# Kernel optimization log

Hardware: AMD Instinct MI355X
Metric: run time of the kernel (lower is better)

## Reference

```python
import jax, jax.numpy as jnp
import numpy as np

B, S, H, D = 2, 2048, 16, 128
HID = H * D  # 2048


def _quantum(x, real, imag, phase, mag):
    # |x * e^{i*phase} * (real + i*imag) * mag| == |x| * sqrt(real^2+imag^2) * |mag|
    # (phase has unit modulus, so it drops out of the magnitude; grad wrt phase is 0,
    # matching torch.abs of the complex product.)
    return jnp.abs(x) * jnp.sqrt(real * real + imag * imag) * jnp.abs(mag)


def setup_inputs() -> dict:
    key = jax.random.key(0)
    ks = jax.random.split(key, 20)
    p = lambda i, shape, s=0.02: jax.random.normal(ks[i], shape, dtype=jnp.float32) * s
    inp = {
        "hidden_states": jax.random.normal(ks[0], (B, S, HID), dtype=jnp.float32),
        "attention_mask": jnp.zeros((B, 1, 1, S), dtype=jnp.float32),
    }
    i = 1
    for name in ("q", "k", "v"):
        inp[name + "_real"] = p(i, (HID,)); i += 1
        inp[name + "_imag"] = p(i, (HID,)); i += 1
        inp[name + "_phase"] = p(i, (HID,), 0.1); i += 1
        inp[name + "_mag"] = jnp.ones((HID,), dtype=jnp.float32)
    for name in ("q", "k", "v", "o"):
        inp["W" + name] = p(i, (HID, HID)); i += 1  # torch Linear weight [out, in]
        inp["b" + name] = jnp.zeros((HID,), dtype=jnp.float32)
    inp["ent"] = p(i, (H, H))
    return inp


def reference(hidden_states, attention_mask,
              q_real, q_imag, q_phase, q_mag,
              k_real, k_imag, k_phase, k_mag,
              v_real, v_imag, v_phase, v_mag,
              Wq, bq, Wk, bk, Wv, bv, Wo, bo, ent):
    Bsz, Sl, _ = hidden_states.shape

    def heads(x):  # [B,S,HID] -> [B,H,S,D]
        return x.reshape(Bsz, Sl, H, D).transpose(0, 2, 1, 3)

    q = heads(_quantum(hidden_states @ Wq.T + bq, q_real, q_imag, q_phase, q_mag))
    k = heads(_quantum(hidden_states @ Wk.T + bk, k_real, k_imag, k_phase, k_mag))
    v = heads(_quantum(hidden_states @ Wv.T + bv, v_real, v_imag, v_phase, v_mag))

    scores = jnp.einsum('bhsd,bhtd->bhst', q, k) / jnp.sqrt(jnp.float32(D))
    # entanglement bias: [H,H] tiled along key axis -> [1,H,1,S]
    bias = jnp.tile(ent, (1, Sl // H))[None, :, None, :]
    scores = scores + bias + attention_mask
    probs = jax.nn.softmax(scores, axis=-1)

    ctx = jnp.einsum('bhst,bhtd->bhsd', probs, v)
    ctx = ctx.transpose(0, 2, 1, 3).reshape(Bsz, Sl, HID)
    return ctx @ Wo.T + bo
```

## Files before the change

kernel.cpp:

```cpp
#include <hip/hip_runtime.h>
#include <hip/hip_bf16.h>

#define NB 2
#define NS 2048
#define NH 16
#define ND 128
#define HID2 2048
#define MROWS 4096

typedef __bf16 bf16;
typedef bf16 bf16x8 __attribute__((ext_vector_type(8)));
typedef bf16 bf16x4 __attribute__((ext_vector_type(4)));
typedef float f32x4 __attribute__((ext_vector_type(4)));
typedef unsigned int u32;

#define GLOBAL_AS __attribute__((address_space(1)))
#define LDS_AS __attribute__((address_space(3)))

__device__ __forceinline__ void async16(void* lds, const void* g) {
    __builtin_amdgcn_global_load_lds((const GLOBAL_AS u32*)g, (LDS_AS u32*)lds, 16, 0, 0);
}

__device__ __forceinline__ void cvt8(const float* __restrict__ src, bf16* __restrict__ dst, int i) {
    const float4* s4 = (const float4*)src;
    float4 a = s4[2 * i], b = s4[2 * i + 1];
    bf16x8 o;
    o[0] = (bf16)a.x; o[1] = (bf16)a.y; o[2] = (bf16)a.z; o[3] = (bf16)a.w;
    o[4] = (bf16)b.x; o[5] = (bf16)b.y; o[6] = (bf16)b.z; o[7] = (bf16)b.w;
    ((bf16x8*)dst)[i] = o;
}

__global__ __launch_bounds__(256) void prep_kernel(
    const float* __restrict__ hidden,
    const float* __restrict__ Wq, const float* __restrict__ Wk,
    const float* __restrict__ Wv, const float* __restrict__ Wo,
    const float* __restrict__ qr, const float* __restrict__ qi, const float* __restrict__ qm,
    const float* __restrict__ kr, const float* __restrict__ ki, const float* __restrict__ km,
    const float* __restrict__ vr, const float* __restrict__ vi, const float* __restrict__ vm,
    bf16* __restrict__ Xb, bf16* __restrict__ Wb, float* __restrict__ scales) {
    int gb = blockIdx.x, tid = threadIdx.x;
    if (gb < 4096) {
        cvt8(hidden, Xb, gb * 256 + tid);
    } else if (gb < 12288) {
        int zz = (gb - 4096) >> 11;
        int i = ((gb - 4096) & 2047) * 256 + tid;
        const float* src = (zz == 0) ? Wq : (zz == 1) ? Wk : (zz == 2) ? Wv : Wo;
        cvt8(src, Wb + (size_t)zz * HID2 * HID2, i);
    } else {
        int i = (gb - 12288) * 256 + tid;
        if (i < HID2) {
            const float RSQD = 0.08838834764831845f;
            scales[i]            = sqrtf(qr[i] * qr[i] + qi[i] * qi[i]) * fabsf(qm[i]) * RSQD;
            scales[HID2 + i]     = sqrtf(kr[i] * kr[i] + ki[i] * ki[i]) * fabsf(km[i]);
            scales[2 * HID2 + i] = sqrtf(vr[i] * vr[i] + vi[i] * vi[i]) * fabsf(vm[i]);
        }
    }
}

__device__ __forceinline__ void stage12(const char* gA, const char* gB,
                                        char* sa, char* sb, int w, int lane, size_t kb) {
    int r8 = lane >> 3;
    int cx = (lane & 7) * 16;
#pragma unroll
    for (int j = 0; j < 4; ++j) {
        int r = w * 32 + j * 8 + r8;
        async16(sa + (w * 32 + j * 8) * 128,
                gA + (size_t)r * (HID2 * 2) + kb + (cx ^ ((r & 7) << 4)));
    }
#pragma unroll
    for (int j = 0; j < 8; ++j) {
        int r = w * 64 + j * 8 + r8;
        async16(sb + (w * 64 + j * 8) * 128,
                gB + (size_t)r * (HID2 * 2) + kb + (cx ^ ((r & 7) << 4)));
    }
}

__global__ __launch_bounds__(256, 2) void gemm_qkv(
    const bf16* __restrict__ X, const bf16* __restrict__ Wb,
    const float* __restrict__ bq, const float* __restrict__ bk, const float* __restrict__ bv,
    const float* __restrict__ scales, bf16* __restrict__ QKV) {
    __shared__ bf16 sA[128 * 64];
    __shared__ bf16 sB[256 * 64];
    int b0 = blockIdx.x;
    int tid = threadIdx.x, w = tid >> 6, lane = tid & 63;
    int wr = w >> 1, wc = w & 1;
    int l15 = lane & 15, l4 = lane >> 4;
    int xorb = (l15 & 7) << 4;
    int ntile = (b0 < 256) ? 2 : 1;

    for (int it = 0; it < ntile; ++it) {
        int t = (it == 0) ? b0 : 512 + b0;
        int p = t & 7, q = t >> 3;
        int z = q >> 5, tm = q & 31, tn = p;
        const bf16* Bt = Wb + (size_t)z * HID2 * HID2;
        const float* bias = (z == 0) ? bq : (z == 1) ? bk : bv;
        const float* scale = scales + z * HID2;
        bf16* Cout = QKV + (size_t)z * MROWS * HID2;

        const char* gA = (const char*)X + (size_t)tm * 128 * (HID2 * 2);
        const char* gB = (const char*)Bt + (size_t)tn * 256 * (HID2 * 2);
        const char* pa = (const char*)sA;
        const char* pb = (const char*)sB;

        f32x4 acc[4][8] = {};

        for (int kt = 0; kt < HID2 / 64; ++kt) {
            stage12(gA, gB, (char*)sA, (char*)sB, w, lane, (size_t)kt * 128);
            __syncthreads();
#pragma unroll
            for (int kk = 0; kk < 2; ++kk) {
                int kc = (kk * 64 + l4 * 16) ^ xorb;
                bf16x8 af[4], bg[4];
#pragma unroll
                for (int m = 0; m < 4; ++m)
                    af[m] = *(const bf16x8*)(pa + (wr * 64 + m * 16 + l15) * 128 + kc);
#pragma unroll
                for (int n = 0; n < 4; ++n)
                    bg[n] = *(const bf16x8*)(pb + (wc * 128 + n * 16 + l15) * 128 + kc);
#pragma unroll
                for (int m = 0; m < 4; ++m)
#pragma unroll
                    for (int n = 0; n < 4; ++n)
                        acc[m][n] = __builtin_amdgcn_mfma_f32_16x16x32_bf16(af[m], bg[n], acc[m][n], 0, 0, 0);
#pragma unroll
                for (int n = 0; n < 4; ++n)
                    bg[n] = *(const bf16x8*)(pb + (wc * 128 + (n + 4) * 16 + l15) * 128 + kc);
#pragma unroll
                for (int m = 0; m < 4; ++m)
#pragma unroll
                    for (int n = 0; n < 4; ++n)
                        acc[m][n + 4] = __builtin_amdgcn_mfma_f32_16x16x32_bf16(af[m], bg[n], acc[m][n + 4], 0, 0, 0);
            }
            __syncthreads();
        }

#pragma unroll
        for (int n = 0; n < 8; ++n) {
            int col = tn * 256 + wc * 128 + n * 16 + l15;
            float bv2 = bias[col];
            float sc = scale[col];
#pragma unroll
            for (int m = 0; m < 4; ++m) {
                int row = tm * 128 + wr * 64 + m * 16 + l4 * 4;
#pragma unroll
                for (int r = 0; r < 4; ++r)
                    Cout[(size_t)(row + r) * HID2 + col] = (bf16)(fabsf(acc[m][n][r] + bv2) * sc);
            }
        }
    }
}

__device__ __forceinline__ void stage2A(const char* gA, char* sa, int w, int lane, size_t kb) {
#pragma unroll
    for (int j = 0; j < 2; ++j) {
        int r = w * 16 + j * 8 + (lane >> 3);
        async16(sa + (w * 16 + j * 8) * 128,
                gA + (size_t)r * (HID2 * 2) + kb + (((lane & 7) * 16) ^ ((r & 7) << 4)));
    }
}
__device__ __forceinline__ void stage2B(const char* gB, char* sb, int w, int lane, int half, size_t kb) {
#pragma unroll
    for (int j = 0; j < 2; ++j) {
        int r = half * 128 + w * 16 + j * 8 + (lane >> 3);
        async16(sb + (half * 128 + w * 16 + j * 8) * 128,
                gB + (size_t)r * (HID2 * 2) + kb + (((lane & 7) * 16) ^ ((r & 7) << 4)));
    }
}

#define G_BARRIER() do { asm volatile("" ::: "memory"); __builtin_amdgcn_s_barrier(); \
                         asm volatile("" ::: "memory"); } while (0)

__global__ __launch_bounds__(512, 2) void gemm_out(
    const bf16* __restrict__ Ctx, const bf16* __restrict__ Wo,
    const float* __restrict__ bo, float* __restrict__ out) {
    __shared__ bf16 sA[3][128 * 64];
    __shared__ bf16 sB[3][256 * 64];
    const int NT = HID2 / 64;
    int bid = blockIdx.x;
    int tn = bid & 7, tm = bid >> 3;
    int tid = threadIdx.x, w = tid >> 6, lane = tid & 63;
    int wr = w >> 2, wc = w & 3;
    int l15 = lane & 15, l4 = lane >> 4;
    int xorb = (l15 & 7) << 4;

    const char* gA = (const char*)Ctx + (size_t)tm * 128 * (HID2 * 2);
    const char* gB = (const char*)Wo + (size_t)tn * 256 * (HID2 * 2);

    f32x4 acc[4][4] = {};

    stage2A(gA, (char*)sA[0], w, lane, 0);
    stage2B(gB, (char*)sB[0], w, lane, 0, 0);
    stage2B(gB, (char*)sB[0], w, lane, 1, 0);
    stage2A(gA, (char*)sA[1], w, lane, 128);
    stage2B(gB, (char*)sB[1], w, lane, 0, 128);
    stage2B(gB, (char*)sB[1], w, lane, 1, 128);
    asm volatile("s_waitcnt vmcnt(6)" ::: "memory");
    G_BARRIER();

    int cur = 0;
    for (int t = 0; t < NT; ++t) {
        const char* pa = (const char*)sA[cur];
        const char* pb = (const char*)sB[cur];
        int nb = cur + 2; if (nb >= 3) nb -= 3;
        const bool pre = (t + 2 < NT);
        size_t kb = (size_t)(t + 2) * 128;
        bf16x8 af[4], bg[4];

        {
            int kc = (l4 * 16) ^ xorb;
#pragma unroll
            for (int m = 0; m < 4; ++m)
                af[m] = *(const bf16x8*)(pa + (wr * 64 + m * 16 + l15) * 128 + kc);
#pragma unroll
            for (int n = 0; n < 4; ++n)
                bg[n] = *(const bf16x8*)(pb + (wc * 64 + n * 16 + l15) * 128 + kc);
        }
        if (pre) { stage2A(gA, (char*)sA[nb], w, lane, kb); stage2B(gB, (char*)sB[nb], w, lane, 0, kb); }
        G_BARRIER();
        asm volatile("s_waitcnt lgkmcnt(0)" ::: "memory");
        __builtin_amdgcn_sched_barrier(0);
        __builtin_amdgcn_s_setprio(1);
#pragma unroll
        for (int m = 0; m < 4; ++m)
#pragma unroll
            for (int n = 0; n < 4; ++n)
                acc[m][n] = __builtin_amdgcn_mfma_f32_16x16x32_bf16(af[m], bg[n], acc[m][n], 0, 0, 0);
        __builtin_amdgcn_s_setprio(0);
        G_BARRIER();

        {
            int kc = (64 + l4 * 16) ^ xorb;
#pragma unroll
            for (int m = 0; m < 4; ++m)
                af[m] = *(const bf16x8*)(pa + (wr * 64 + m * 16 + l15) * 128 + kc);
#pragma unroll
            for (int n = 0; n < 4; ++n)
                bg[n] = *(const bf16x8*)(pb + (wc * 64 + n * 16 + l15) * 128 + kc);
        }
        if (pre) stage2B(gB, (char*)sB[nb], w, lane, 1, kb);
        G_BARRIER();
        asm volatile("s_waitcnt lgkmcnt(0)" ::: "memory");
        __builtin_amdgcn_sched_barrier(0);
        __builtin_amdgcn_s_setprio(1);
#pragma unroll
        for (int m = 0; m < 4; ++m)
#pragma unroll
            for (int n = 0; n < 4; ++n)
                acc[m][n] = __builtin_amdgcn_mfma_f32_16x16x32_bf16(af[m], bg[n], acc[m][n], 0, 0, 0);
        __builtin_amdgcn_s_setprio(0);
        if (pre)               { asm volatile("s_waitcnt vmcnt(6)" ::: "memory"); }
        else if (t + 2 == NT)  { asm volatile("s_waitcnt vmcnt(0)" ::: "memory"); }
        G_BARRIER();

        cur = cur + 1; if (cur == 3) cur = 0;
    }

#pragma unroll
    for (int n = 0; n < 4; ++n) {
        int col = tn * 256 + wc * 64 + n * 16 + l15;
        float bv = bo[col];
#pragma unroll
        for (int m = 0; m < 4; ++m) {
            int row = tm * 128 + wr * 64 + m * 16 + l4 * 4;
#pragma unroll
            for (int r = 0; r < 4; ++r)
                out[(size_t)(row + r) * HID2 + col] = acc[m][n][r] + bv;
        }
    }
}

__global__ void transpose_v(const bf16* __restrict__ Vb, bf16* __restrict__ Vt) {
    int bh = blockIdx.z;
    int b = bh >> 4, h = bh & 15;
    int s0 = blockIdx.x * 64, d0 = blockIdx.y * 64;
    int tid = threadIdx.x;
    __shared__ bf16 T[64][72];
    const bf16* src = Vb + ((size_t)b * NS + s0) * HID2 + h * ND + d0;
#pragma unroll
    for (int i = 0; i < 2; ++i) {
        int r = i * 32 + (tid >> 3);
        int c = (tid & 7) * 8;
        *(bf16x8*)(&T[r][c]) = *(const bf16x8*)(src + (size_t)r * HID2 + c);
    }
    __syncthreads();
    bf16* dst = Vt + ((size_t)(b * NH + h) * ND + d0) * NS + s0;
#pragma unroll
    for (int i = 0; i < 2; ++i) {
        int dr = i * 32 + (tid >> 3);
        int sc = (tid & 7) * 8;
        bf16x8 o;
#pragma unroll
        for (int j = 0; j < 8; ++j) o[j] = T[sc + j][dr];
        *(bf16x8*)(dst + (size_t)dr * NS + sc) = o;
    }
}

__device__ __forceinline__ void stage_load(const bf16* __restrict__ Kp, const bf16* __restrict__ Vp,
                                           int kt, int tid, bf16x8 kreg[4], bf16x8 vreg[4]) {
#pragma unroll
    for (int i = 0; i < 4; ++i) {
        kreg[i] = *(const bf16x8*)(Kp + (size_t)(kt * 64 + i * 16 + (tid >> 4)) * HID2 + (tid & 15) * 8);
        vreg[i] = *(const bf16x8*)(Vp + (size_t)(i * 32 + (tid >> 3)) * NS + kt * 64 + (tid & 7) * 8);
    }
}

__global__ __launch_bounds__(256, 2) void flash_kernel(
    const bf16* __restrict__ Qb, const bf16* __restrict__ Kb, const bf16* __restrict__ Vt,
    const float* __restrict__ ent, const float* __restrict__ mask, bf16* __restrict__ Ctx) {
    int bid = blockIdx.x;
    int qt = bid >> 5;
    int bh = (bid & 7) * 4 + ((bid >> 3) & 3);
    int b = bh >> 4, h = bh & 15;
    int tid = threadIdx.x, wid = tid >> 6, lane = tid & 63;
    int l15 = lane & 15, l4 = lane >> 4;

    __shared__ bf16 Ks[64 * 136];
    __shared__ bf16 Vs[128 * 72];
    __shared__ bf16 Ps[4][32 * 72];

    const bf16* Qp = Qb + ((size_t)b * NS + qt * 128) * HID2 + h * ND;
    const bf16* Kp = Kb + (size_t)b * NS * HID2 + h * ND;
    const bf16* Vp = Vt + (size_t)(b * NH + h) * ND * NS;
    const float* maskp = mask + (size_t)b * NS;

    bf16x8 qf[2][4];
#pragma unroll
    for (int m = 0; m < 2; ++m)
#pragma unroll
        for (int kk = 0; kk < 4; ++kk)
            qf[m][kk] = *(const bf16x8*)(Qp + (size_t)(wid * 32 + m * 16 + l15) * HID2 + kk * 32 + l4 * 8);

    float eb[4];
#pragma unroll
    for (int r = 0; r < 4; ++r) eb[r] = ent[h * NH + l4 * 4 + r];

    float mrun[2], lrun[2];
    mrun[0] = mrun[1] = -INFINITY;
    lrun[0] = lrun[1] = 0.f;
    f32x4 oacc[2][8] = {};

    bf16x8 kreg[4], vreg[4];
    stage_load(Kp, Vp, 0, tid, kreg, vreg);
#pragma unroll
    for (int i = 0; i < 4; ++i) {
        *(bf16x8*)(&Ks[(i * 16 + (tid >> 4)) * 136 + (tid & 15) * 8]) = kreg[i];
        *(bf16x8*)(&Vs[(i * 32 + (tid >> 3)) * 72 + (tid & 7) * 8]) = vreg[i];
    }

    for (int kt = 0; kt < NS / 64; ++kt) {
        __syncthreads();
        if (kt + 1 < NS / 64) stage_load(Kp, Vp, kt + 1, tid, kreg, vreg);

        f32x4 s[2][4] = {};
#pragma unroll
        for (int kk = 0; kk < 4; ++kk) {
            bf16x8 kf[4];
#pragma unroll
            for (int n = 0; n < 4; ++n)
                kf[n] = *(const bf16x8*)(&Ks[(n * 16 + l15) * 136 + kk * 32 + l4 * 8]);
#pragma unroll
            for (int m = 0; m < 2; ++m)
#pragma unroll
                for (int n = 0; n < 4; ++n)
                    s[m][n] = __builtin_amdgcn_mfma_f32_16x16x32_bf16(kf[n], qf[m][kk], s[m][n], 0, 0, 0);
        }

        float4 mk[4];
#pragma unroll
        for (int n = 0; n < 4; ++n)
            mk[n] = *(const float4*)(maskp + kt * 64 + n * 16 + l4 * 4);

#pragma unroll
        for (int mq = 0; mq < 2; ++mq) {
            float sv[4][4];
#pragma unroll
            for (int n = 0; n < 4; ++n) {
                sv[n][0] = s[mq][n][0] + eb[0] + mk[n].x;
                sv[n][1] = s[mq][n][1] + eb[1] + mk[n].y;
                sv[n][2] = s[mq][n][2] + eb[2] + mk[n].z;
                sv[n][3] = s[mq][n][3] + eb[3] + mk[n].w;
            }
            float tmax = sv[0][0];
#pragma unroll
            for (int n = 0; n < 4; ++n)
#pragma unroll
                for (int r = 0; r < 4; ++r) tmax = fmaxf(tmax, sv[n][r]);
            tmax = fmaxf(tmax, __shfl_xor(tmax, 16));
            tmax = fmaxf(tmax, __shfl_xor(tmax, 32));

            if (__any(tmax > mrun[mq] + 8.0f)) {
                float mnew = fmaxf(mrun[mq], tmax);
                float corr = __expf(mrun[mq] - mnew);
                mrun[mq] = mnew;
                lrun[mq] *= corr;
#pragma unroll
                for (int r = 0; r < 4; ++r) {
                    float cr = __shfl(corr, l4 * 4 + r);
#pragma unroll
                    for (int n = 0; n < 8; ++n) oacc[mq][n][r] *= cr;
                }
            }

            float psum = 0.f;
#pragma unroll
            for (int n = 0; n < 4; ++n) {
                bf16x4 pv;
#pragma unroll
                for (int r = 0; r < 4; ++r) {
                    float p = __expf(sv[n][r] - mrun[mq]);
                    psum += p;
                    pv[r] = (bf16)p;
                }
                *(bf16x4*)(&Ps[wid][(mq * 16 + l15) * 72 + n * 16 + l4 * 4]) = pv;
            }
            psum += __shfl_xor(psum, 16);
            psum += __shfl_xor(psum, 32);
            lrun[mq] += psum;
        }

#pragma unroll
        for (int kk = 0; kk < 2; ++kk) {
            bf16x8 pa[2], vb[8];
#pragma unroll
            for (int m = 0; m < 2; ++m)
                pa[m] = *(const bf16x8*)(&Ps[wid][(m * 16 + l15) * 72 + kk * 32 + l4 * 8]);
#pragma unroll
            for (int n = 0; n < 8; ++n)
                vb[n] = *(const bf16x8*)(&Vs[(n * 16 + l15) * 72 + kk * 32 + l4 * 8]);
#pragma unroll
            for (int m = 0; m < 2; ++m)
#pragma unroll
                for (int n = 0; n < 8; ++n)
                    oacc[m][n] = __builtin_amdgcn_mfma_f32_16x16x32_bf16(pa[m], vb[n], oacc[m][n], 0, 0, 0);
        }
        __syncthreads();
        if (kt + 1 < NS / 64) {
#pragma unroll
            for (int i = 0; i < 4; ++i) {
                *(bf16x8*)(&Ks[(i * 16 + (tid >> 4)) * 136 + (tid & 15) * 8]) = kreg[i];
                *(bf16x8*)(&Vs[(i * 32 + (tid >> 3)) * 72 + (tid & 7) * 8]) = vreg[i];
            }
        }
    }

#pragma unroll
    for (int m = 0; m < 2; ++m) {
        float inv = 1.0f / lrun[m];
        float invr[4];
#pragma unroll
        for (int r = 0; r < 4; ++r) invr[r] = __shfl(inv, l4 * 4 + r);
#pragma unroll
        for (int r = 0; r < 4; ++r) {
            int row = qt * 128 + wid * 32 + m * 16 + l4 * 4 + r;
            bf16* Cp = Ctx + ((size_t)b * NS + row) * HID2 + h * ND;
#pragma unroll
            for (int n = 0; n < 8; ++n)
                Cp[n * 16 + l15] = (bf16)(oacc[m][n][r] * invr[r]);
        }
    }
}

extern "C" void kernel_launch(void* const* d_in, const int* in_sizes, int n_in,
                              void* d_out, int out_size, void* d_ws, size_t ws_size,
                              hipStream_t stream) {
    const float* hidden = (const float*)d_in[0];
    const float* mask   = (const float*)d_in[1];
    const float* q_real = (const float*)d_in[2];
    const float* q_imag = (const float*)d_in[3];
    const float* q_mag  = (const float*)d_in[5];
    const float* k_real = (const float*)d_in[6];
    const float* k_imag = (const float*)d_in[7];
    const float* k_mag  = (const float*)d_in[9];
    const float* v_real = (const float*)d_in[10];
    const float* v_imag = (const float*)d_in[11];
    const float* v_mag  = (const float*)d_in[13];
    const float* Wq = (const float*)d_in[14];
    const float* bq = (const float*)d_in[15];
    const float* Wk = (const float*)d_in[16];
    const float* bk = (const float*)d_in[17];
    const float* Wv = (const float*)d_in[18];
    const float* bv = (const float*)d_in[19];
    const float* Wo = (const float*)d_in[20];
    const float* bo = (const float*)d_in[21];
    const float* ent = (const float*)d_in[22];

    char* ws = (char*)d_ws;
    bf16* Xb    = (bf16*)(ws);
    bf16* Wb    = (bf16*)(ws + 16777216);
    bf16* Wob   = (bf16*)(ws + 41943040);
    bf16* QKV   = (bf16*)(ws + 50331648);
    bf16* Vt    = (bf16*)(ws + 100663296);
    bf16* Ctx   = (bf16*)(ws + 117440512);
    float* scales = (float*)(ws + 134217728);

    prep_kernel<<<12296, 256, 0, stream>>>(hidden, Wq, Wk, Wv, Wo,
                                           q_real, q_imag, q_mag, k_real, k_imag, k_mag,
                                           v_real, v_imag, v_mag, Xb, Wb, scales);
    gemm_qkv<<<512, 256, 0, stream>>>(Xb, Wb, bq, bk, bv, scales, QKV);
    const bf16* Vb = QKV + (size_t)2 * MROWS * HID2;
    transpose_v<<<dim3(32, 2, 32), 256, 0, stream>>>(Vb, Vt);
    flash_kernel<<<512, 256, 0, stream>>>(QKV, QKV + (size_t)MROWS * HID2, Vt, ent, mask, Ctx);
    gemm_out<<<256, 512, 0, stream>>>(Ctx, Wob, bo, (float*)d_out);
}
```

Measured before the change: 283.5 us.

## Double-buffer K/V tiles via async global-to-LDS loads with XOR swizzle

The flash attention kernel now streams K and V tiles straight into LDS with async global_load_lds, replacing the register-staged loads and stores. It double-buffers those tiles so the next tile loads while the current one is computed. It also drops the padded LDS layouts for K, V and P in favour of an XOR-swizzled layout to avoid bank conflicts. This is meant to cut register pressure and the store pass through registers. The cost is more LDS use per block (two K/V buffers), which may lower occupancy at two blocks per CU.

```diff
diff --git a/kernel.cpp b/kernel.cpp
--- a/kernel.cpp
+++ b/kernel.cpp
@@ -295,12 +295,17 @@
     }
 }
 
-__device__ __forceinline__ void stage_load(const bf16* __restrict__ Kp, const bf16* __restrict__ Vp,
-                                           int kt, int tid, bf16x8 kreg[4], bf16x8 vreg[4]) {
+__device__ __forceinline__ void stageKV(const char* Kp, const char* Vp,
+                                        char* ksDst, char* vsDst, int w, int lane) {
 #pragma unroll
     for (int i = 0; i < 4; ++i) {
-        kreg[i] = *(const bf16x8*)(Kp + (size_t)(kt * 64 + i * 16 + (tid >> 4)) * HID2 + (tid & 15) * 8);
-        vreg[i] = *(const bf16x8*)(Vp + (size_t)(i * 32 + (tid >> 3)) * NS + kt * 64 + (tid & 7) * 8);
+        int c = (w * 4 + i) * 64 + lane;
+        int key = c >> 4, s16 = c & 15;
+        async16(ksDst + (size_t)(w * 4 + i) * 1024,
+                Kp + (size_t)key * (HID2 * 2) + (((s16 ^ (key & 7)) << 4)));
+        int d = c >> 3, s8 = c & 7;
+        async16(vsDst + (size_t)(w * 4 + i) * 1024,
+                Vp + (size_t)d * (NS * 2) + (((s8 ^ (d & 7)) << 4)));
     }
 }
 
@@ -313,14 +318,15 @@
     int b = bh >> 4, h = bh & 15;
     int tid = threadIdx.x, wid = tid >> 6, lane = tid & 63;
     int l15 = lane & 15, l4 = lane >> 4;
-
-    __shared__ bf16 Ks[64 * 136];
-    __shared__ bf16 Vs[128 * 72];
-    __shared__ bf16 Ps[4][32 * 72];
+    int xorb = (l15 & 7) << 4;
+
+    __shared__ bf16 Ks[2][64 * 128];
+    __shared__ bf16 Vs[2][128 * 64];
+    __shared__ bf16 Ps[4][32 * 64];
 
     const bf16* Qp = Qb + ((size_t)b * NS + qt * 128) * HID2 + h * ND;
-    const bf16* Kp = Kb + (size_t)b * NS * HID2 + h * ND;
-    const bf16* Vp = Vt + (size_t)(b * NH + h) * ND * NS;
+    const char* Kp = (const char*)(Kb + (size_t)b * NS * HID2 + h * ND);
+    const char* Vp = (const char*)(Vt + (size_t)(b * NH + h) * ND * NS);
     const float* maskp = mask + (size_t)b * NS;
 
     bf16x8 qf[2][4];
@@ -339,17 +345,18 @@
     lrun[0] = lrun[1] = 0.f;
     f32x4 oacc[2][8] = {};
 
-    bf16x8 kreg[4], vreg[4];
-    stage_load(Kp, Vp, 0, tid, kreg, vreg);
-#pragma unroll
-    for (int i = 0; i < 4; ++i) {
-        *(bf16x8*)(&Ks[(i * 16 + (tid >> 4)) * 136 + (tid & 15) * 8]) = kreg[i];
-        *(bf16x8*)(&Vs[(i * 32 + (tid >> 3)) * 72 + (tid & 7) * 8]) = vreg[i];
-    }
+    stageKV(Kp, Vp, (char*)Ks[0], (char*)Vs[0], wid, lane);
+    __syncthreads();
 
     for (int kt = 0; kt < NS / 64; ++kt) {
-        __syncthreads();
-        if (kt + 1 < NS / 64) stage_load(Kp, Vp, kt + 1, tid, kreg, vreg);
+        int kb = kt & 1;
+        if (kt + 1 < NS / 64)
+            stageKV(Kp + (size_t)(kt + 1) * 64 * (HID2 * 2), Vp + (size_t)(kt + 1) * 128,
+                    (char*)Ks[kb ^ 1], (char*)Vs[kb ^ 1], wid, lane);
+
+        const char* ks = (const char*)Ks[kb];
+        const char* vs = (const char*)Vs[kb];
+        const char* ps = (const char*)Ps[wid];
 
         f32x4 s[2][4] = {};
 #pragma unroll
@@ -357,7 +364,7 @@
             bf16x8 kf[4];
 #pragma unroll
             for (int n = 0; n < 4; ++n)
-                kf[n] = *(const bf16x8*)(&Ks[(n * 16 + l15) * 136 + kk * 32 + l4 * 8]);
+                kf[n] = *(const bf16x8*)(ks + (n * 16 + l15) * 256 + ((kk * 64 + l4 * 16) ^ xorb));
 #pragma unroll
             for (int m = 0; m < 2; ++m)
 #pragma unroll
@@ -411,7 +418,7 @@
                     psum += p;
                     pv[r] = (bf16)p;
                 }
-                *(bf16x4*)(&Ps[wid][(mq * 16 + l15) * 72 + n * 16 + l4 * 4]) = pv;
+                *(bf16x4*)((char*)ps + (mq * 16 + l15) * 128 + ((n * 32 + l4 * 8) ^ xorb)) = pv;
             }
             psum += __shfl_xor(psum, 16);
             psum += __shfl_xor(psum, 32);
@@ -423,10 +430,10 @@
             bf16x8 pa[2], vb[8];
 #pragma unroll
             for (int m = 0; m < 2; ++m)
-                pa[m] = *(const bf16x8*)(&Ps[wid][(m * 16 + l15) * 72 + kk * 32 + l4 * 8]);
+                pa[m] = *(const bf16x8*)(ps + (m * 16 + l15) * 128 + ((kk * 64 + l4 * 16) ^ xorb));
 #pragma unroll
             for (int n = 0; n < 8; ++n)
-                vb[n] = *(const bf16x8*)(&Vs[(n * 16 + l15) * 72 + kk * 32 + l4 * 8]);
+                vb[n] = *(const bf16x8*)(vs + (n * 16 + l15) * 128 + ((kk * 64 + l4 * 16) ^ xorb));
 #pragma unroll
             for (int m = 0; m < 2; ++m)
 #pragma unroll
@@ -434,13 +441,6 @@
                     oacc[m][n] = __builtin_amdgcn_mfma_f32_16x16x32_bf16(pa[m], vb[n], oacc[m][n], 0, 0, 0);
         }
         __syncthreads();
-        if (kt + 1 < NS / 64) {
-#pragma unroll
-            for (int i = 0; i < 4; ++i) {
-                *(bf16x8*)(&Ks[(i * 16 + (tid >> 4)) * 136 + (tid & 15) * 8]) = kreg[i];
-                *(bf16x8*)(&Vs[(i * 32 + (tid >> 3)) * 72 + (tid & 7) * 8]) = vreg[i];
-            }
-        }
     }
 
 #pragma unroll
```

Result: no change. 280.3 us (-1.1%).
